# Optimization experiments

Measured on AMD Instinct MI355X. Metric: run time of the kernel, lower is better.

## Reference

```python
import jax, jax.numpy as jnp
import numpy as np

N, E, IN, ED, HID, HEADS, OUT, G = 50000, 800000, 128, 16, 32, 4, 64, 64
NEG_SLOPE = 0.2


def gat_conv(x, src, dst, edge_attr, W, att_src, att_dst, We, att_edge, bias,
             heads, out_ch, concat):
    """PyG-style GATConv with edge attributes and mean-filled self loops.
    src/dst already include self loops; edge_attr already includes fill rows."""
    n = x.shape[0]
    h = (x @ W).reshape(n, heads, out_ch)                      # [N,H,C]
    a_src = jnp.einsum('nhc,hc->nh', h, att_src)               # [N,H]
    a_dst = jnp.einsum('nhc,hc->nh', h, att_dst)
    eh = (edge_attr @ We).reshape(-1, heads, out_ch)           # [E',H,C]
    a_edge = jnp.einsum('ehc,hc->eh', eh, att_edge)            # [E',H]
    alpha = jax.nn.leaky_relu(a_src[src] + a_dst[dst] + a_edge, NEG_SLOPE)
    # segment softmax over incoming edges of each target node
    amax = jax.ops.segment_max(alpha, dst, num_segments=n)
    ex = jnp.exp(alpha - amax[dst])
    denom = jax.ops.segment_sum(ex, dst, num_segments=n)
    coef = ex / (denom[dst] + 1e-16)                           # [E',H]
    msg = h[src] * coef[:, :, None]                            # [E',H,C]
    out = jax.ops.segment_sum(msg, dst, num_segments=n)        # [N,H,C]
    out = out.reshape(n, heads * out_ch) if concat else out.mean(axis=1)
    return out + bias


def add_self_loops(edge_index, edge_attr, n):
    loop = jnp.arange(n, dtype=edge_index.dtype)
    src = jnp.concatenate([edge_index[0], loop])
    dst = jnp.concatenate([edge_index[1], loop])
    fill = jnp.broadcast_to(edge_attr.mean(axis=0), (n, edge_attr.shape[1]))
    ea = jnp.concatenate([edge_attr, fill], axis=0)
    return src, dst, ea


def setup_inputs() -> dict:
    key = jax.random.key(0)
    ks = jax.random.split(key, 16)
    s1 = 1.0 / np.sqrt(IN)
    s2 = 1.0 / np.sqrt(HID * HEADS)
    se = 1.0 / np.sqrt(ED)
    return {
        'x': jax.random.normal(ks[0], (N, IN), jnp.float32),
        'edge_index': jax.random.randint(ks[1], (2, E), 0, N, jnp.int64),
        'edge_attr': jax.random.normal(ks[2], (E, ED), jnp.float32),
        'batch': jnp.sort(jax.random.randint(ks[3], (N,), 0, G, jnp.int64)),
        # layer 1 params (heads=4, concat=True)
        'W1': jax.random.normal(ks[4], (IN, HEADS * HID), jnp.float32) * s1,
        'att_src1': jax.random.normal(ks[5], (HEADS, HID), jnp.float32) * s1,
        'att_dst1': jax.random.normal(ks[6], (HEADS, HID), jnp.float32) * s1,
        'We1': jax.random.normal(ks[7], (ED, HEADS * HID), jnp.float32) * se,
        'att_edge1': jax.random.normal(ks[8], (HEADS, HID), jnp.float32) * se,
        'b1': jnp.zeros((HEADS * HID,), jnp.float32),
        # layer 2 params (heads=1, concat=False)
        'W2': jax.random.normal(ks[9], (HEADS * HID, OUT), jnp.float32) * s2,
        'att_src2': jax.random.normal(ks[10], (1, OUT), jnp.float32) * s2,
        'att_dst2': jax.random.normal(ks[11], (1, OUT), jnp.float32) * s2,
        'We2': jax.random.normal(ks[12], (ED, OUT), jnp.float32) * se,
        'att_edge2': jax.random.normal(ks[13], (1, OUT), jnp.float32) * se,
        'b2': jnp.zeros((OUT,), jnp.float32),
    }


def reference(x, edge_index, edge_attr, batch,
              W1, att_src1, att_dst1, We1, att_edge1, b1,
              W2, att_src2, att_dst2, We2, att_edge2, b2):
    src, dst, ea = add_self_loops(edge_index, edge_attr, x.shape[0])
    h = gat_conv(x, src, dst, ea, W1, att_src1, att_dst1, We1, att_edge1, b1,
                 HEADS, HID, concat=True)
    h = jax.nn.elu(h)
    h = gat_conv(h, src, dst, ea, W2, att_src2, att_dst2, We2, att_edge2, b2,
                 1, OUT, concat=False)
    # global mean pool over graphs
    sums = jax.ops.segment_sum(h, batch, num_segments=G)
    cnts = jax.ops.segment_sum(jnp.ones((h.shape[0],), h.dtype), batch, num_segments=G)
    return sums / jnp.maximum(cnts, 1.0)[:, None]
```

## Files before the change

### kernel.cpp

```cpp
#include <hip/hip_runtime.h>
#include <hip/hip_fp16.h>
#include <math.h>

#define NN 50000
#define NE 800000
#define EDF 16
#define C1 128
#define HID 32
#define OUTF 64
#define NG 64
#define SLOPE 0.2f
#define NB 196
#define MAXE 256
#define PB 256
#define PCH 196
#define SEB 512
#define HB 3125
#define G1B 1563
#define G2B 1563

static inline int cdiv(long a, long b){ return (int)((a + b - 1) / b); }

__device__ __forceinline__ float lrelu(float x){ return x >= 0.f ? x : SLOPE * x; }

typedef _Float16 f16x8 __attribute__((ext_vector_type(8)));
typedef float f32x4 __attribute__((ext_vector_type(4)));
#define MFMA16(a, b, c) __builtin_amdgcn_mfma_f32_16x16x32_f16((a), (b), (c), 0, 0, 0)

__global__ __launch_bounds__(256) void k_pre(const float* __restrict__ ea,
                                             float* __restrict__ part,
                                             const int* __restrict__ dst,
                                             int* __restrict__ deg,
                                             int* __restrict__ rank){
  int b = blockIdx.x;
  int t = threadIdx.x;
  if (b < SEB){
    const float4* ea4 = (const float4*)ea;
    const long total = (long)NE * 4;
    const long stride = (long)SEB * 256;
    float4 acc = make_float4(0.f, 0.f, 0.f, 0.f);
    for (long i = (long)b * 256 + t; i < total; i += stride * 4){
      float4 a0 = make_float4(0,0,0,0), a1 = a0, a2 = a0, a3 = a0;
      long i1 = i + stride, i2 = i + 2*stride, i3 = i + 3*stride;
      a0 = ea4[i];
      if (i1 < total) a1 = ea4[i1];
      if (i2 < total) a2 = ea4[i2];
      if (i3 < total) a3 = ea4[i3];
      acc.x += a0.x + a1.x + a2.x + a3.x;
      acc.y += a0.y + a1.y + a2.y + a3.y;
      acc.z += a0.z + a1.z + a2.z + a3.z;
      acc.w += a0.w + a1.w + a2.w + a3.w;
    }
    __shared__ float4 sp[256];
    sp[t] = acc;
    __syncthreads();
    for (int st = 128; st >= 4; st >>= 1){
      if (t < st){
        sp[t].x += sp[t+st].x; sp[t].y += sp[t+st].y;
        sp[t].z += sp[t+st].z; sp[t].w += sp[t+st].w;
      }
      __syncthreads();
    }
    if (t < 4) *(float4*)&part[b * 16 + t * 4] = sp[t];
  } else {
    long e = (long)(b - SEB) * 256 + t;
    if (e < NE) rank[e] = atomicAdd(&deg[dst[e]], 1);
  }
}

__global__ void k_scan1(const int* __restrict__ deg, int* __restrict__ rowStart,
                        int* __restrict__ blockSums,
                        const float* __restrict__ We1, const float* __restrict__ att_e1,
                        const float* __restrict__ We2, const float* __restrict__ att_e2,
                        const float* __restrict__ part,
                        float* __restrict__ M1, float* __restrict__ M2,
                        float* __restrict__ aeSL1, float* __restrict__ aeSL2,
                        const float* __restrict__ W1, const float* __restrict__ W2,
                        __half* __restrict__ W1Th, __half* __restrict__ W1Tl,
                        __half* __restrict__ W2Th, __half* __restrict__ W2Tl){
  int t = threadIdx.x;
  int bid = blockIdx.x;
  if (bid > NB){
    int wchunk = bid - NB - 1;
    if (wchunk < 64){
      int i = wchunk * 256 + t;
      int c = i & 127, k = i >> 7;
      float w = W1[i];
      __half h = __float2half_rn(w);
      W1Th[c * 128 + k] = h;
      W1Tl[c * 128 + k] = __float2half_rn((w - __half2float(h)) * 4096.0f);
    } else {
      int i = (wchunk - 64) * 256 + t;
      int c = i & 63, k = i >> 6;
      float w = W2[i];
      __half h = __float2half_rn(w);
      W2Th[c * 128 + k] = h;
      W2Tl[c * 128 + k] = __float2half_rn((w - __half2float(h)) * 4096.0f);
    }
    return;
  }
  if (bid == NB){
    __shared__ float red[256];
    __shared__ float sMean[16];
    __shared__ float sM1p[64];
    __shared__ float sM2p[16];
    {
      int c = t & 15, q = t >> 4;
      float s0 = 0.f;
      for (int b = q; b < SEB; b += 16) s0 += part[b * 16 + c];
      red[t] = s0;
    }
    if (t < 64){
      int h = t >> 4, d = t & 15;
      float s = 0.f;
      for (int cc = 0; cc < HID; cc++) s += We1[d * C1 + h * HID + cc] * att_e1[h * HID + cc];
      M1[h * 16 + d] = s; sM1p[t] = s;
    }
    if (t >= 64 && t < 80){
      int d = t - 64;
      float s = 0.f;
      for (int cc = 0; cc < OUTF; cc++) s += We2[d * OUTF + cc] * att_e2[cc];
      M2[d] = s; sM2p[d] = s;
    }
    __syncthreads();
    if (t < 16){
      float m = 0.f;
      for (int q2 = 0; q2 < 16; q2++) m += red[q2 * 16 + t];
      sMean[t] = m * (1.0f / NE);
    }
    __syncthreads();
    if (t < 4){
      float s = 0.f;
      for (int d = 0; d < 16; d++) s += sMean[d] * sM1p[t * 16 + d];
      aeSL1[t] = s;
    }
    if (t == 4){
      float s = 0.f;
      for (int d = 0; d < 16; d++) s += sMean[d] * sM2p[d];
      *aeSL2 = s;
    }
    return;
  }
  __shared__ int sd[256];
  int i = bid * 256 + t;
  int v = (i < NN) ? deg[i] : 0;
  sd[t] = v;
  __syncthreads();
  for (int off = 1; off < 256; off <<= 1){
    int add = (t >= off) ? sd[t - off] : 0;
    __syncthreads();
    sd[t] += add;
    __syncthreads();
  }
  int incl = sd[t];
  if (i < NN) rowStart[i] = incl - v;
  if (t == 255) blockSums[bid] = incl;
}

__global__ void k_scan3(int* __restrict__ rowStart, const int* __restrict__ blockSums){
  __shared__ int sp[256];
  int t = threadIdx.x;
  int bid = blockIdx.x;
  sp[t] = (t < bid) ? blockSums[t] : 0;
  __syncthreads();
  for (int st = 128; st >= 1; st >>= 1){
    if (t < st) sp[t] += sp[t + st];
    __syncthreads();
  }
  int prefix = sp[0];
  int i = bid * 256 + t;
  if (i < NN) rowStart[i] += prefix;
  if (i == 0) rowStart[NN] = NE;
}

__global__ __launch_bounds__(256) void k_sg(
    const int* __restrict__ src, const int* __restrict__ dst,
    const float* __restrict__ ea, const int* __restrict__ rowStart,
    const int* __restrict__ rank,
    const float* __restrict__ M1, const float* __restrict__ M2,
    unsigned int* __restrict__ recC,
    const float* __restrict__ x,
    const __half* __restrict__ W1Th, const __half* __restrict__ W1Tl,
    __half* __restrict__ Ch,
    const float* __restrict__ attS, const float* __restrict__ attD,
    float* __restrict__ aS, float* __restrict__ aD){
  __shared__ __align__(16) __half Ash[4096];
  __shared__ __align__(16) __half Asl[4096];
  __shared__ float sM[80];
  int t = threadIdx.x;
  if ((int)blockIdx.x >= G1B){
    if (t < 64) sM[t] = M1[t];
    if (t >= 64 && t < 80) sM[t] = M2[t - 64];
    __syncthreads();
    long e = (long)(blockIdx.x - G1B) * 256 + t;
    if (e >= NE) return;
    int d = dst[e];
    int s = src[e];
    int rk = rank[e];
    float eav[16];
    const float4* p = (const float4*)(ea + e * EDF);
    *(float4*)&eav[0]  = p[0]; *(float4*)&eav[4]  = p[1];
    *(float4*)&eav[8]  = p[2]; *(float4*)&eav[12] = p[3];
    int pos = rowStart[d] + rk;
    float ae[4];
#pragma unroll
    for (int h = 0; h < 4; h++){
      float sdot = 0.f;
#pragma unroll
      for (int dd = 0; dd < 16; dd++) sdot += eav[dd] * sM[h * 16 + dd];
      ae[h] = sdot;
    }
    float a2 = 0.f;
#pragma unroll
    for (int dd = 0; dd < 16; dd++) a2 += eav[dd] * sM[64 + dd];
    __half2 ae01 = __floats2half2_rn(ae[0], ae[1]);
    __half2 ae23 = __floats2half2_rn(ae[2], ae[3]);
    __half  a2h  = __float2half_rn(a2);
    uint4 rec;
    rec.x = (unsigned)s | ((unsigned)*(unsigned short*)&a2h << 16);
    rec.y = *(unsigned*)&ae01;
    rec.z = *(unsigned*)&ae23;
    rec.w = 0u;
    *(uint4*)&recC[(long)pos * 4] = rec;
    return;
  }
  int row0 = blockIdx.x * 32;
  {
    int srow = t >> 3, sseg = t & 7;
    int gr = row0 + srow;
    float xv[16];
    if (gr < NN){
      const float4* xp = (const float4*)(x + (long)gr * 128 + sseg * 16);
      *(float4*)&xv[0]  = xp[0]; *(float4*)&xv[4]  = xp[1];
      *(float4*)&xv[8]  = xp[2]; *(float4*)&xv[12] = xp[3];
    } else {
#pragma unroll
      for (int i = 0; i < 16; i++) xv[i] = 0.f;
    }
    f16x8 vh[2], vl[2];
#pragma unroll
    for (int q = 0; q < 2; q++)
#pragma unroll
      for (int i = 0; i < 8; i++){
        float f = xv[q * 8 + i];
        _Float16 h = (_Float16)f;
        vh[q][i] = h;
        vl[q][i] = (_Float16)(f - (float)h);
      }
    int sb = srow * 256 + sseg * 32;
    int sw = (srow & 7) << 4;
    *(f16x8*)((char*)Ash + ((sb     ) ^ sw)) = vh[0];
    *(f16x8*)((char*)Ash + ((sb + 16) ^ sw)) = vh[1];
    *(f16x8*)((char*)Asl + ((sb     ) ^ sw)) = vl[0];
    *(f16x8*)((char*)Asl + ((sb + 16) ^ sw)) = vl[1];
  }
  __syncthreads();
  int wave = t >> 6, lane = t & 63, g = lane >> 4, li = lane & 15;
  const f16x8* BhP = (const f16x8*)W1Th;
  const f16x8* BlP = (const f16x8*)W1Tl;
  int c0 = wave * 32 + li;
  int c1 = c0 + 16;
  f32x4 z = {0.f, 0.f, 0.f, 0.f};
  f32x4 aM00 = z, aM01 = z, aM10 = z, aM11 = z;
  f32x4 aL00 = z, aL01 = z, aL10 = z, aL11 = z;
  int ro0 = li * 256, ro1 = (16 + li) * 256;
  int sw0 = (li & 7) << 4;
#pragma unroll
  for (int ks = 0; ks < 4; ks++){
    int ko = ks * 64 + g * 16;
    f16x8 ah0 = *(const f16x8*)((char*)Ash + ((ro0 + ko) ^ sw0));
    f16x8 ah1 = *(const f16x8*)((char*)Ash + ((ro1 + ko) ^ sw0));
    f16x8 al0 = *(const f16x8*)((char*)Asl + ((ro0 + ko) ^ sw0));
    f16x8 al1 = *(const f16x8*)((char*)Asl + ((ro1 + ko) ^ sw0));
    f16x8 bh0 = BhP[c0 * 16 + ks * 4 + g];
    f16x8 bh1 = BhP[c1 * 16 + ks * 4 + g];
    f16x8 bl0 = BlP[c0 * 16 + ks * 4 + g];
    f16x8 bl1 = BlP[c1 * 16 + ks * 4 + g];
    aM00 = MFMA16(ah0, bh0, aM00); aM01 = MFMA16(ah0, bh1, aM01);
    aM10 = MFMA16(ah1, bh0, aM10); aM11 = MFMA16(ah1, bh1, aM11);
    aM00 = MFMA16(al0, bh0, aM00); aM01 = MFMA16(al0, bh1, aM01);
    aM10 = MFMA16(al1, bh0, aM10); aM11 = MFMA16(al1, bh1, aM11);
    aL00 = MFMA16(ah0, bl0, aL00); aL01 = MFMA16(ah0, bl1, aL01);
    aL10 = MFMA16(ah1, bl0, aL10); aL11 = MFMA16(ah1, bl1, aL11);
  }
  const float s = 1.0f / 4096.0f;
  f32x4 D00 = aM00 + aL00 * s, D01 = aM01 + aL01 * s;
  f32x4 D10 = aM10 + aL10 * s, D11 = aM11 + aL11 * s;
  float avS0 = attS[c0], avS1 = attS[c1];
  float avD0 = attD[c0], avD1 = attD[c1];
  float ssv[2][4], sdv[2][4];
#pragma unroll
  for (int r = 0; r < 4; r++){
    ssv[0][r] = D00[r] * avS0 + D01[r] * avS1;
    ssv[1][r] = D10[r] * avS0 + D11[r] * avS1;
    sdv[0][r] = D00[r] * avD0 + D01[r] * avD1;
    sdv[1][r] = D10[r] * avD0 + D11[r] * avD1;
  }
#pragma unroll
  for (int off = 1; off <= 8; off <<= 1)
#pragma unroll
    for (int mt = 0; mt < 2; mt++)
#pragma unroll
      for (int r = 0; r < 4; r++){
        ssv[mt][r] += __shfl_xor(ssv[mt][r], off);
        sdv[mt][r] += __shfl_xor(sdv[mt][r], off);
      }
  __syncthreads();
  __half* sOut = Ash;
#pragma unroll
  for (int mt = 0; mt < 2; mt++)
#pragma unroll
    for (int r = 0; r < 4; r++){
      int rl = mt * 16 + g * 4 + r;
      sOut[rl * 128 + c0] = __float2half_rn(mt ? D10[r] : D00[r]);
      sOut[rl * 128 + c1] = __float2half_rn(mt ? D11[r] : D01[r]);
    }
  if (li == 0){
#pragma unroll
    for (int mt = 0; mt < 2; mt++)
#pragma unroll
      for (int r = 0; r < 4; r++){
        int grow = row0 + mt * 16 + g * 4 + r;
        if (grow < NN){
          aS[(long)grow * 4 + wave] = ssv[mt][r];
          aD[(long)grow * 4 + wave] = sdv[mt][r];
        }
      }
  }
  __syncthreads();
  {
    int row = t >> 3, seg = t & 7;
    int grw = row0 + row;
    if (grw < NN){
      uint4 u0 = *(uint4*)&sOut[row * 128 + seg * 16];
      uint4 u1 = *(uint4*)&sOut[row * 128 + seg * 16 + 8];
      *(uint4*)&Ch[(long)grw * 128 + seg * 16] = u0;
      *(uint4*)&Ch[(long)grw * 128 + seg * 16 + 8] = u1;
    }
  }
}

__global__ __launch_bounds__(256) void k_gemm2(
    const __half* __restrict__ Ahp,
    const __half* __restrict__ W2Th, const __half* __restrict__ W2Tl,
    __half* __restrict__ Ch,
    const float* __restrict__ attS, const float* __restrict__ attD,
    float* __restrict__ aS, float* __restrict__ aD){
  __shared__ __align__(16) __half As[4096];
  __shared__ float sRS[128], sRD[128];
  int t = threadIdx.x;
  int row0 = blockIdx.x * 32;
  {
    int srow = t >> 3, sseg = t & 7;
    int gr = row0 + srow;
    uint4 u0 = {0,0,0,0}, u1 = {0,0,0,0};
    if (gr < NN){
      const uint4* p = (const uint4*)(Ahp + (long)gr * 128 + sseg * 16);
      u0 = p[0]; u1 = p[1];
    }
    int sb = srow * 256 + sseg * 32;
    int sw = (srow & 7) << 4;
    *(uint4*)((char*)As + ((sb     ) ^ sw)) = u0;
    *(uint4*)((char*)As + ((sb + 16) ^ sw)) = u1;
  }
  __syncthreads();
  int wave = t >> 6, lane = t & 63, g = lane >> 4, li = lane & 15;
  int cw = wave * 16 + li;
  const f16x8* BhP = (const f16x8*)W2Th;
  const f16x8* BlP = (const f16x8*)W2Tl;
  f32x4 z = {0.f, 0.f, 0.f, 0.f};
  f32x4 aM0 = z, aM1 = z, aL0 = z, aL1 = z;
  int ro0 = li * 256, ro1 = (16 + li) * 256, sw0 = (li & 7) << 4;
#pragma unroll
  for (int ks = 0; ks < 4; ks++){
    int ko = ks * 64 + g * 16;
    f16x8 a0 = *(const f16x8*)((char*)As + ((ro0 + ko) ^ sw0));
    f16x8 a1 = *(const f16x8*)((char*)As + ((ro1 + ko) ^ sw0));
    f16x8 bh = BhP[cw * 16 + ks * 4 + g];
    f16x8 bl = BlP[cw * 16 + ks * 4 + g];
    aM0 = MFMA16(a0, bh, aM0); aM1 = MFMA16(a1, bh, aM1);
    aL0 = MFMA16(a0, bl, aL0); aL1 = MFMA16(a1, bl, aL1);
  }
  const float s = 1.0f / 4096.0f;
  f32x4 D0 = aM0 + aL0 * s, D1 = aM1 + aL1 * s;
  float avS = attS[cw], avD = attD[cw];
  float ssv[2][4], sdv[2][4];
#pragma unroll
  for (int r = 0; r < 4; r++){
    ssv[0][r] = D0[r] * avS; ssv[1][r] = D1[r] * avS;
    sdv[0][r] = D0[r] * avD; sdv[1][r] = D1[r] * avD;
  }
#pragma unroll
  for (int off = 1; off <= 8; off <<= 1)
#pragma unroll
    for (int mt = 0; mt < 2; mt++)
#pragma unroll
      for (int r = 0; r < 4; r++){
        ssv[mt][r] += __shfl_xor(ssv[mt][r], off);
        sdv[mt][r] += __shfl_xor(sdv[mt][r], off);
      }
  __syncthreads();
  __half* sOut = As;
#pragma unroll
  for (int mt = 0; mt < 2; mt++)
#pragma unroll
    for (int r = 0; r < 4; r++){
      int rl = mt * 16 + g * 4 + r;
      sOut[rl * 64 + cw] = __float2half_rn(mt ? D1[r] : D0[r]);
      if (li == 0){
        sRS[wave * 32 + rl] = ssv[mt][r];
        sRD[wave * 32 + rl] = sdv[mt][r];
      }
    }
  __syncthreads();
  if (t < 32){
    int grow = row0 + t;
    if (grow < NN){
      aS[grow] = sRS[t] + sRS[32 + t] + sRS[64 + t] + sRS[96 + t];
      aD[grow] = sRD[t] + sRD[32 + t] + sRD[64 + t] + sRD[96 + t];
    }
  }
  {
    int row = t >> 3, seg = t & 7;
    int grw = row0 + row;
    if (grw < NN)
      *(uint4*)&Ch[(long)grw * 64 + seg * 8] = *(uint4*)&sOut[row * 64 + seg * 8];
  }
}

__global__ __launch_bounds__(256) void k_agg1(
    const int* __restrict__ rowStart, const unsigned int* __restrict__ recC,
    const float* __restrict__ a_src, const float* __restrict__ a_dst,
    const float* __restrict__ aeSL1,
    const __half* __restrict__ h1h, const float* __restrict__ b1,
    __half* __restrict__ out1h){
  __shared__ int   sS[4][MAXE];
  __shared__ float sC[4][MAXE * 4];
  int wid = threadIdx.x >> 6;
  int lane = threadIdx.x & 63;
  int n = blockIdx.x * 4 + wid;
  int start = rowStart[n];
  int dg = rowStart[n + 1] - start;
  float4 sl4 = *(const float4*)aeSL1;
  float4 ad4 = *(const float4*)(a_dst + (long)n * 4);
  float4 as4 = *(const float4*)(a_src + (long)n * 4);
  float4 cSelf;
  cSelf.x = __expf(lrelu(as4.x + ad4.x + sl4.x));
  cSelf.y = __expf(lrelu(as4.y + ad4.y + sl4.y));
  cSelf.z = __expf(lrelu(as4.z + ad4.z + sl4.z));
  cSelf.w = __expf(lrelu(as4.w + ad4.w + sl4.w));
  float4 dsum = make_float4(0.f, 0.f, 0.f, 0.f);
  for (int j0 = 0; j0 < dg; j0 += 64){
    int j = j0 + lane;
    if (j < dg){
      uint4 rec = *(const uint4*)&recC[(long)(start + j) * 4];
      int s = rec.x & 0xffff;
      float2 ae01 = __half22float2(*(__half2*)&rec.y);
      float2 ae23 = __half22float2(*(__half2*)&rec.z);
      float4 asv = *(const float4*)(a_src + (long)s * 4);
      float4 c;
      c.x = __expf(lrelu(asv.x + ad4.x + ae01.x));
      c.y = __expf(lrelu(asv.y + ad4.y + ae01.y));
      c.z = __expf(lrelu(asv.z + ad4.z + ae23.x));
      c.w = __expf(lrelu(asv.w + ad4.w + ae23.y));
      dsum.x += c.x; dsum.y += c.y; dsum.z += c.z; dsum.w += c.w;
      if (j < MAXE){
        sS[wid][j] = s << 6;
        *(float4*)&sC[wid][j * 4] = c;
      }
    }
  }
#pragma unroll
  for (int off = 32; off > 0; off >>= 1){
    dsum.x += __shfl_xor(dsum.x, off);
    dsum.y += __shfl_xor(dsum.y, off);
    dsum.z += __shfl_xor(dsum.z, off);
    dsum.w += __shfl_xor(dsum.w, off);
  }
  float adA[4] = {ad4.x, ad4.y, ad4.z, ad4.w};
  float csA[4] = {cSelf.x, cSelf.y, cSelf.z, cSelf.w};
  float invA[4];
  invA[0] = 1.f / (dsum.x + cSelf.x + 1e-16f);
  invA[1] = 1.f / (dsum.y + cSelf.y + 1e-16f);
  invA[2] = 1.f / (dsum.z + cSelf.z + 1e-16f);
  invA[3] = 1.f / (dsum.w + cSelf.w + 1e-16f);
  int ch = lane * 2;
  int h = lane >> 4;
  const unsigned int* hrow = (const unsigned int*)h1h;
  float cs   = csA[h];
  float vinv = invA[h];
  float adh  = adA[h];
  unsigned int hv = hrow[(unsigned)(n * 64 + lane)];
  float2 hf = __half22float2(*(__half2*)&hv);
  float acc0 = hf.x * cs, acc1 = hf.y * cs;
  int jmax = dg < MAXE ? dg : MAXE;
  int j = 0;
  for (; j + 4 <= jmax; j += 4){
    int o0 = sS[wid][j+0], o1 = sS[wid][j+1], o2 = sS[wid][j+2], o3 = sS[wid][j+3];
    float c0 = sC[wid][(j+0)*4+h], c1 = sC[wid][(j+1)*4+h];
    float c2 = sC[wid][(j+2)*4+h], c3 = sC[wid][(j+3)*4+h];
    unsigned int v0 = hrow[(unsigned)(o0 + lane)];
    unsigned int v1 = hrow[(unsigned)(o1 + lane)];
    unsigned int v2 = hrow[(unsigned)(o2 + lane)];
    unsigned int v3 = hrow[(unsigned)(o3 + lane)];
    float2 f0 = __half22float2(*(__half2*)&v0);
    float2 f1 = __half22float2(*(__half2*)&v1);
    float2 f2 = __half22float2(*(__half2*)&v2);
    float2 f3 = __half22float2(*(__half2*)&v3);
    acc0 += c0 * f0.x + c1 * f1.x + c2 * f2.x + c3 * f3.x;
    acc1 += c0 * f0.y + c1 * f1.y + c2 * f2.y + c3 * f3.y;
  }
  for (; j < jmax; j++){
    int o = sS[wid][j];
    float c = sC[wid][j * 4 + h];
    unsigned int v = hrow[(unsigned)(o + lane)];
    float2 f = __half22float2(*(__half2*)&v);
    acc0 += c * f.x; acc1 += c * f.y;
  }
  for (; j < dg; j++){
    uint4 rec = *(const uint4*)&recC[(long)(start + j) * 4];
    int s = rec.x & 0xffff;
    float2 ae01 = __half22float2(*(__half2*)&rec.y);
    float2 ae23 = __half22float2(*(__half2*)&rec.z);
    float aeA[4] = {ae01.x, ae01.y, ae23.x, ae23.y};
    float asv = a_src[(long)s * 4 + h];
    float c = __expf(lrelu(asv + adh + aeA[h]));
    unsigned int v = hrow[(unsigned)((s << 6) + lane)];
    float2 f = __half22float2(*(__half2*)&v);
    acc0 += c * f.x; acc1 += c * f.y;
  }
  float v0 = acc0 * vinv + b1[ch];
  float v1 = acc1 * vinv + b1[ch + 1];
  v0 = v0 > 0.f ? v0 : __expf(v0) - 1.f;
  v1 = v1 > 0.f ? v1 : __expf(v1) - 1.f;
  __half2 pk = __floats2half2_rn(v0, v1);
  ((unsigned int*)out1h)[(unsigned)(n * 64 + lane)] = *(unsigned*)&pk;
}

__global__ __launch_bounds__(256) void k_agg2(
    const int* __restrict__ rowStart, const unsigned int* __restrict__ recC,
    const float* __restrict__ a_src, const float* __restrict__ a_dst,
    const float* __restrict__ aeSL2,
    const __half* __restrict__ h2h, float* __restrict__ out2){
  __shared__ int   sS[4][MAXE];
  __shared__ float sC[4][MAXE];
  int wid = threadIdx.x >> 6;
  int lane = threadIdx.x & 63;
  int n = blockIdx.x * 4 + wid;
  int start = rowStart[n];
  int dg = rowStart[n + 1] - start;
  float adN = a_dst[n];
  float cSelf = __expf(lrelu(a_src[n] + adN + *aeSL2));
  float dsum = 0.f;
  for (int j0 = 0; j0 < dg; j0 += 64){
    int j = j0 + lane;
    if (j < dg){
      unsigned rx = recC[(long)(start + j) * 4];
      int s = rx & 0xffff;
      unsigned short ah = (unsigned short)(rx >> 16);
      float c = __expf(lrelu(a_src[s] + adN + __half2float(*(__half*)&ah)));
      dsum += c;
      if (j < MAXE){ sS[wid][j] = s << 6; sC[wid][j] = c; }
    }
  }
#pragma unroll
  for (int off = 32; off > 0; off >>= 1) dsum += __shfl_xor(dsum, off);
  float inv = 1.f / (dsum + cSelf + 1e-16f);
  float acc = __half2float(h2h[(unsigned)(n * 64 + lane)]) * cSelf;
  int jmax = dg < MAXE ? dg : MAXE;
  int j = 0;
  for (; j + 4 <= jmax; j += 4){
    int o0 = sS[wid][j+0], o1 = sS[wid][j+1], o2 = sS[wid][j+2], o3 = sS[wid][j+3];
    float c0 = sC[wid][j+0], c1 = sC[wid][j+1], c2 = sC[wid][j+2], c3 = sC[wid][j+3];
    float f0 = __half2float(h2h[(unsigned)(o0 + lane)]);
    float f1 = __half2float(h2h[(unsigned)(o1 + lane)]);
    float f2 = __half2float(h2h[(unsigned)(o2 + lane)]);
    float f3 = __half2float(h2h[(unsigned)(o3 + lane)]);
    acc += c0 * f0 + c1 * f1 + c2 * f2 + c3 * f3;
  }
  for (; j < jmax; j++)
    acc += sC[wid][j] * __half2float(h2h[(unsigned)(sS[wid][j] + lane)]);
  for (; j < dg; j++){
    unsigned rx = recC[(long)(start + j) * 4];
    int s = rx & 0xffff;
    unsigned short ah = (unsigned short)(rx >> 16);
    float c = __expf(lrelu(a_src[s] + adN + __half2float(*(__half*)&ah)));
    acc += c * __half2float(h2h[(unsigned)((s << 6) + lane)]);
  }
  out2[(long)n * OUTF + lane] = acc * inv;
}

__global__ __launch_bounds__(256) void k_pool1(const float* __restrict__ out2,
                                               const int* __restrict__ batch,
                                               float* __restrict__ gsum){
  int c = threadIdx.x & 63, r = threadIdx.x >> 6;
  int n0 = blockIdx.x * PCH + r;
  int n1 = blockIdx.x * PCH + PCH; if (n1 > NN) n1 = NN;
  float acc = 0.f; int curG = -1;
  for (int n = n0; n < n1; n += 4){
    int g = batch[n];
    if (g != curG){
      if (curG >= 0) atomicAdd(&gsum[curG * 64 + c], acc);
      curG = g; acc = 0.f;
    }
    acc += out2[(long)n * OUTF + c];
  }
  if (curG >= 0) atomicAdd(&gsum[curG * 64 + c], acc);
}

__global__ void k_pool2(const float* __restrict__ gsum, const int* __restrict__ batch,
                        const float* __restrict__ b2, float* __restrict__ out){
  int g = blockIdx.x;
  int c = threadIdx.x;
  int lo = 0, hi = NN;
  while (lo < hi){ int mid = (lo + hi) >> 1; if (batch[mid] < g) lo = mid + 1; else hi = mid; }
  int a = lo, b = NN;
  while (a < b){ int mid = (a + b) >> 1; if (batch[mid] < g + 1) a = mid + 1; else b = mid; }
  int cnt = a - lo;
  out[g * 64 + c] = (gsum[g * 64 + c] + (float)cnt * b2[c]) / fmaxf((float)cnt, 1.0f);
}

extern "C" void kernel_launch(void* const* d_in, const int* in_sizes, int n_in,
                              void* d_out, int out_size, void* d_ws, size_t ws_size,
                              hipStream_t stream) {
  const float* x         = (const float*)d_in[0];
  const int*   eidx      = (const int*)d_in[1];
  const float* edge_attr = (const float*)d_in[2];
  const int*   batch     = (const int*)d_in[3];
  const float* W1        = (const float*)d_in[4];
  const float* att_src1  = (const float*)d_in[5];
  const float* att_dst1  = (const float*)d_in[6];
  const float* We1       = (const float*)d_in[7];
  const float* att_edge1 = (const float*)d_in[8];
  const float* b1        = (const float*)d_in[9];
  const float* W2        = (const float*)d_in[10];
  const float* att_src2  = (const float*)d_in[11];
  const float* att_dst2  = (const float*)d_in[12];
  const float* We2       = (const float*)d_in[13];
  const float* att_edge2 = (const float*)d_in[14];
  const float* b2        = (const float*)d_in[15];
  const int* srcI = eidx;
  const int* dstI = eidx + NE;

  float* ws = (float*)d_ws;
  __half* h1h   = (__half*)ws;
  __half* out1h = (__half*)(ws + 3200000);
  float* out2   = ws + 6400000;
  float* a_src1 = ws + 9600000;
  float* a_dst1 = a_src1 + (long)NN * 4;
  unsigned int* recC = (unsigned int*)(a_dst1 + (long)NN * 4);
  int*   deg    = (int*)(recC + (long)NE * 4);
  float* gsum   = (float*)(deg + NN);
  int*   rowStart = (int*)(gsum + NG * 64);
  int*   blockSums = rowStart + 50004;
  float* part   = (float*)(blockSums + 260);
  float* M1     = part + SEB * 16;
  float* M2v    = M1 + 64;
  float* aeSL1  = M2v + 16;
  float* aeSL2  = aeSL1 + 4;
  int*   rank   = (int*)(aeSL2 + 4);
  __half* W1Th  = (__half*)(rank + NE);
  __half* W1Tl  = W1Th + 16384;
  __half* W2Th  = W1Tl + 16384;
  __half* W2Tl  = W2Th + 8192;
  __half* h2h = h1h;
  float* a_src2 = a_src1; float* a_dst2 = a_dst1;

  hipMemsetAsync(deg, 0, (NN + NG * 64) * sizeof(int), stream);
  k_pre<<<SEB + HB, 256, 0, stream>>>(edge_attr, part, dstI, deg, rank);
  k_scan1<<<NB + 97, 256, 0, stream>>>(deg, rowStart, blockSums,
                                       We1, att_edge1, We2, att_edge2, part,
                                       M1, M2v, aeSL1, aeSL2,
                                       W1, W2, W1Th, W1Tl, W2Th, W2Tl);
  k_scan3<<<NB, 256, 0, stream>>>(rowStart, blockSums);
  k_sg<<<G1B + HB, 256, 0, stream>>>(srcI, dstI, edge_attr, rowStart, rank,
                                     M1, M2v, recC,
                                     x, W1Th, W1Tl, h1h, att_src1, att_dst1,
                                     a_src1, a_dst1);
  k_agg1<<<NN / 4, 256, 0, stream>>>(rowStart, recC, a_src1, a_dst1, aeSL1,
                                     h1h, b1, out1h);
  k_gemm2<<<G2B, 256, 0, stream>>>(out1h, W2Th, W2Tl, h2h, att_src2, att_dst2,
                                   a_src2, a_dst2);
  k_agg2<<<NN / 4, 256, 0, stream>>>(rowStart, recC, a_src2, a_dst2, aeSL2,
                                     h2h, out2);
  k_pool1<<<PB, 256, 0, stream>>>(out2, batch, gsum);
  k_pool2<<<NG, 64, 0, stream>>>(gsum, batch, b2, (float*)d_out);
}
```

Baseline: 319.5 us.

## Fuse edge-attr projection and mean partials into degree-count pre-pass

```diff
diff --git a/kernel.cpp b/kernel.cpp
--- a/kernel.cpp
+++ b/kernel.cpp
@@ -14,7 +14,6 @@
 #define MAXE 256
 #define PB 256
 #define PCH 196
-#define SEB 512
 #define HB 3125
 #define G1B 1563
 #define G2B 1563
@@ -27,45 +26,77 @@
 typedef float f32x4 __attribute__((ext_vector_type(4)));
 #define MFMA16(a, b, c) __builtin_amdgcn_mfma_f32_16x16x32_f16((a), (b), (c), 0, 0, 0)
 
-__global__ __launch_bounds__(256) void k_pre(const float* __restrict__ ea,
-                                             float* __restrict__ part,
-                                             const int* __restrict__ dst,
-                                             int* __restrict__ deg,
-                                             int* __restrict__ rank){
-  int b = blockIdx.x;
+__global__ __launch_bounds__(256) void k_pre(
+    const float* __restrict__ ea,
+    const int* __restrict__ src, const int* __restrict__ dst,
+    const float* __restrict__ We1, const float* __restrict__ att_e1,
+    const float* __restrict__ We2, const float* __restrict__ att_e2,
+    int* __restrict__ deg,
+    unsigned int* __restrict__ recE,
+    float* __restrict__ part){
+  __shared__ float sM[80];
+  __shared__ float sWS[64];
   int t = threadIdx.x;
-  if (b < SEB){
-    const float4* ea4 = (const float4*)ea;
-    const long total = (long)NE * 4;
-    const long stride = (long)SEB * 256;
-    float4 acc = make_float4(0.f, 0.f, 0.f, 0.f);
-    for (long i = (long)b * 256 + t; i < total; i += stride * 4){
-      float4 a0 = make_float4(0,0,0,0), a1 = a0, a2 = a0, a3 = a0;
-      long i1 = i + stride, i2 = i + 2*stride, i3 = i + 3*stride;
-      a0 = ea4[i];
-      if (i1 < total) a1 = ea4[i1];
-      if (i2 < total) a2 = ea4[i2];
-      if (i3 < total) a3 = ea4[i3];
-      acc.x += a0.x + a1.x + a2.x + a3.x;
-      acc.y += a0.y + a1.y + a2.y + a3.y;
-      acc.z += a0.z + a1.z + a2.z + a3.z;
-      acc.w += a0.w + a1.w + a2.w + a3.w;
-    }
-    __shared__ float4 sp[256];
-    sp[t] = acc;
-    __syncthreads();
-    for (int st = 128; st >= 4; st >>= 1){
-      if (t < st){
-        sp[t].x += sp[t+st].x; sp[t].y += sp[t+st].y;
-        sp[t].z += sp[t+st].z; sp[t].w += sp[t+st].w;
-      }
-      __syncthreads();
-    }
-    if (t < 4) *(float4*)&part[b * 16 + t * 4] = sp[t];
+  if (t < 64){
+    int h = t >> 4, d = t & 15;
+    float s = 0.f;
+    for (int c = 0; c < HID; c++) s += We1[d * C1 + h * HID + c] * att_e1[h * HID + c];
+    sM[t] = s;
+  }
+  if (t >= 64 && t < 80){
+    int d = t - 64;
+    float s = 0.f;
+    for (int c = 0; c < OUTF; c++) s += We2[d * OUTF + c] * att_e2[c];
+    sM[t] = s;
+  }
+  __syncthreads();
+  long e = (long)blockIdx.x * 256 + t;
+  float eav[16];
+  bool valid = e < NE;
+  if (valid){
+    const float4* p = (const float4*)(ea + e * EDF);
+    *(float4*)&eav[0]  = p[0]; *(float4*)&eav[4]  = p[1];
+    *(float4*)&eav[8]  = p[2]; *(float4*)&eav[12] = p[3];
   } else {
-    long e = (long)(b - SEB) * 256 + t;
-    if (e < NE) rank[e] = atomicAdd(&deg[dst[e]], 1);
-  }
+#pragma unroll
+    for (int i = 0; i < 16; i++) eav[i] = 0.f;
+  }
+  if (valid){
+    float ae[4];
+#pragma unroll
+    for (int h = 0; h < 4; h++){
+      float sdot = 0.f;
+#pragma unroll
+      for (int dd = 0; dd < 16; dd++) sdot += eav[dd] * sM[h * 16 + dd];
+      ae[h] = sdot;
+    }
+    float a2 = 0.f;
+#pragma unroll
+    for (int dd = 0; dd < 16; dd++) a2 += eav[dd] * sM[64 + dd];
+    int d = dst[e];
+    int s = src[e];
+    unsigned rk = (unsigned)atomicAdd(&deg[d], 1);
+    __half2 ae01 = __floats2half2_rn(ae[0], ae[1]);
+    __half2 ae23 = __floats2half2_rn(ae[2], ae[3]);
+    __half  a2h  = __float2half_rn(a2);
+    uint4 rec;
+    rec.x = (unsigned)s | ((unsigned)*(unsigned short*)&a2h << 16);
+    rec.y = *(unsigned*)&ae01;
+    rec.z = *(unsigned*)&ae23;
+    rec.w = rk;
+    *(uint4*)&recE[e * 4] = rec;
+  }
+  int lane = t & 63, wid = t >> 6;
+#pragma unroll
+  for (int c = 0; c < 16; c++){
+    float v = eav[c];
+#pragma unroll
+    for (int off = 32; off > 0; off >>= 1) v += __shfl_xor(v, off);
+    if (lane == 0) sWS[wid * 16 + c] = v;
+  }
+  __syncthreads();
+  if (t < 16)
+    part[blockIdx.x * 16 + t] = sWS[t] + sWS[16 + t] + sWS[32 + t] + sWS[48 + t];
 }
 
 __global__ void k_scan1(const int* __restrict__ deg, int* __restrict__ rowStart,
@@ -73,7 +104,6 @@
                         const float* __restrict__ We1, const float* __restrict__ att_e1,
                         const float* __restrict__ We2, const float* __restrict__ att_e2,
                         const float* __restrict__ part,
-                        float* __restrict__ M1, float* __restrict__ M2,
                         float* __restrict__ aeSL1, float* __restrict__ aeSL2,
                         const float* __restrict__ W1, const float* __restrict__ W2,
                         __half* __restrict__ W1Th, __half* __restrict__ W1Tl,
@@ -107,20 +137,20 @@
     {
       int c = t & 15, q = t >> 4;
       float s0 = 0.f;
-      for (int b = q; b < SEB; b += 16) s0 += part[b * 16 + c];
+      for (int b = q; b < HB; b += 16) s0 += part[b * 16 + c];
       red[t] = s0;
     }
     if (t < 64){
       int h = t >> 4, d = t & 15;
       float s = 0.f;
       for (int cc = 0; cc < HID; cc++) s += We1[d * C1 + h * HID + cc] * att_e1[h * HID + cc];
-      M1[h * 16 + d] = s; sM1p[t] = s;
+      sM1p[t] = s;
     }
     if (t >= 64 && t < 80){
       int d = t - 64;
       float s = 0.f;
       for (int cc = 0; cc < OUTF; cc++) s += We2[d * OUTF + cc] * att_e2[cc];
-      M2[d] = s; sM2p[d] = s;
+      sM2p[d] = s;
     }
     __syncthreads();
     if (t < 16){
@@ -174,10 +204,9 @@
 }
 
 __global__ __launch_bounds__(256) void k_sg(
-    const int* __restrict__ src, const int* __restrict__ dst,
-    const float* __restrict__ ea, const int* __restrict__ rowStart,
-    const int* __restrict__ rank,
-    const float* __restrict__ M1, const float* __restrict__ M2,
+    const int* __restrict__ dst,
+    const unsigned int* __restrict__ recE,
+    const int* __restrict__ rowStart,
     unsigned int* __restrict__ recC,
     const float* __restrict__ x,
     const __half* __restrict__ W1Th, const __half* __restrict__ W1Tl,
@@ -186,41 +215,13 @@
     float* __restrict__ aS, float* __restrict__ aD){
   __shared__ __align__(16) __half Ash[4096];
   __shared__ __align__(16) __half Asl[4096];
-  __shared__ float sM[80];
   int t = threadIdx.x;
   if ((int)blockIdx.x >= G1B){
-    if (t < 64) sM[t] = M1[t];
-    if (t >= 64 && t < 80) sM[t] = M2[t - 64];
-    __syncthreads();
     long e = (long)(blockIdx.x - G1B) * 256 + t;
     if (e >= NE) return;
+    uint4 rec = *(const uint4*)&recE[e * 4];
     int d = dst[e];
-    int s = src[e];
-    int rk = rank[e];
-    float eav[16];
-    const float4* p = (const float4*)(ea + e * EDF);
-    *(float4*)&eav[0]  = p[0]; *(float4*)&eav[4]  = p[1];
-    *(float4*)&eav[8]  = p[2]; *(float4*)&eav[12] = p[3];
-    int pos = rowStart[d] + rk;
-    float ae[4];
-#pragma unroll
-    for (int h = 0; h < 4; h++){
-      float sdot = 0.f;
-#pragma unroll
-      for (int dd = 0; dd < 16; dd++) sdot += eav[dd] * sM[h * 16 + dd];
-      ae[h] = sdot;
-    }
-    float a2 = 0.f;
-#pragma unroll
-    for (int dd = 0; dd < 16; dd++) a2 += eav[dd] * sM[64 + dd];
-    __half2 ae01 = __floats2half2_rn(ae[0], ae[1]);
-    __half2 ae23 = __floats2half2_rn(ae[2], ae[3]);
-    __half  a2h  = __float2half_rn(a2);
-    uint4 rec;
-    rec.x = (unsigned)s | ((unsigned)*(unsigned short*)&a2h << 16);
-    rec.y = *(unsigned*)&ae01;
-    rec.z = *(unsigned*)&ae23;
-    rec.w = 0u;
+    int pos = rowStart[d] + (int)rec.w;
     *(uint4*)&recC[(long)pos * 4] = rec;
     return;
   }
@@ -654,12 +655,10 @@
   int*   rowStart = (int*)(gsum + NG * 64);
   int*   blockSums = rowStart + 50004;
   float* part   = (float*)(blockSums + 260);
-  float* M1     = part + SEB * 16;
-  float* M2v    = M1 + 64;
-  float* aeSL1  = M2v + 16;
+  float* aeSL1  = part + (long)HB * 16;
   float* aeSL2  = aeSL1 + 4;
-  int*   rank   = (int*)(aeSL2 + 4);
-  __half* W1Th  = (__half*)(rank + NE);
+  unsigned int* recE = (unsigned int*)(aeSL2 + 4);
+  __half* W1Th  = (__half*)(recE + (long)NE * 4);
   __half* W1Tl  = W1Th + 16384;
   __half* W2Th  = W1Tl + 16384;
   __half* W2Tl  = W2Th + 8192;
@@ -667,14 +666,15 @@
   float* a_src2 = a_src1; float* a_dst2 = a_dst1;
 
   hipMemsetAsync(deg, 0, (NN + NG * 64) * sizeof(int), stream);
-  k_pre<<<SEB + HB, 256, 0, stream>>>(edge_attr, part, dstI, deg, rank);
+  k_pre<<<HB, 256, 0, stream>>>(edge_attr, srcI, dstI,
+                                We1, att_edge1, We2, att_edge2,
+                                deg, recE, part);
   k_scan1<<<NB + 97, 256, 0, stream>>>(deg, rowStart, blockSums,
                                        We1, att_edge1, We2, att_edge2, part,
-                                       M1, M2v, aeSL1, aeSL2,
+                                       aeSL1, aeSL2,
                                        W1, W2, W1Th, W1Tl, W2Th, W2Tl);
   k_scan3<<<NB, 256, 0, stream>>>(rowStart, blockSums);
-  k_sg<<<G1B + HB, 256, 0, stream>>>(srcI, dstI, edge_attr, rowStart, rank,
-                                     M1, M2v, recC,
+  k_sg<<<G1B + HB, 256, 0, stream>>>(dstI, recE, rowStart, recC,
                                      x, W1Th, W1Tl, h1h, att_src1, att_dst1,
                                      a_src1, a_dst1);
   k_agg1<<<NN / 4, 256, 0, stream>>>(rowStart, recC, a_src1, a_dst1, aeSL1,
```

New measurement: 352.5 us. 1.1x slower.
